# Kernel tuning notes

Measured on AMD Instinct MI355X. Metric: run time of the kernel, lower is better.

Reference implementation:

```python
import jax, jax.numpy as jnp
import numpy as np

N_AST, M, C, D, H, OUT = 200000, 400000, 25000, 256, 4, 256


def setup_inputs() -> dict:
    key = jax.random.key(0)
    ks = jax.random.split(key, 12)
    s = 0.02
    return {
        "ast_nodes_encodings": jax.random.normal(ks[0], (N_AST, D), jnp.float32),
        "ast_node_idx_to_pdg_node_idx_mapping_key": jax.random.randint(ks[1], (M,), 0, N_AST),
        "ast_node_idx_to_pdg_node_idx_mapping_value": jax.random.randint(ks[2], (M,), 0, C),
        "pdg_node_idx_to_sub_ast_root_idx_mapping_key": jax.random.randint(ks[3], (C,), 0, C),
        "pdg_node_idx_to_sub_ast_root_idx_mapping_value": jax.random.randint(ks[4], (C,), 0, N_AST),
        "nr_cfg_nodes": C,
        "Wq": jax.random.normal(ks[5], (D, D), jnp.float32) * s,
        "bq": jnp.zeros((D,), jnp.float32),
        "Wk": jax.random.normal(ks[6], (D, D), jnp.float32) * s,
        "bk": jnp.zeros((D,), jnp.float32),
        "Wv": jax.random.normal(ks[7], (D, D), jnp.float32) * s,
        "bv": jnp.zeros((D,), jnp.float32),
        "Wo": jax.random.normal(ks[8], (D, OUT), jnp.float32) * s,
        "bo": jnp.zeros((OUT,), jnp.float32),
    }


def _scatter_attn(x, attn_keys, seg, num_segments, Wq, bq, Wk, bk, Wv, bv, Wo, bo):
    # x: [M, D] scattered inputs; attn_keys: [C, D] per-segment queries; seg: [M] segment ids.
    d_h = D // H
    q = (attn_keys @ Wq + bq).reshape(num_segments, H, d_h)  # [C,H,dh]
    k = (x @ Wk + bk).reshape(-1, H, d_h)                    # [M,H,dh]
    v = (x @ Wv + bv).reshape(-1, H, d_h)                    # [M,H,dh]
    scale = 1.0 / jnp.sqrt(jnp.asarray(d_h, x.dtype))
    scores = jnp.einsum('mhd,mhd->mh', k, q[seg]) * scale    # [M,H]
    m = jax.ops.segment_max(scores, seg, num_segments=num_segments)  # [C,H]
    e = jnp.exp(scores - m[seg])                             # [M,H]
    denom = jax.ops.segment_sum(e, seg, num_segments=num_segments)  # [C,H]
    num = jax.ops.segment_sum((e[..., None] * v).reshape(-1, H * d_h),
                              seg, num_segments=num_segments)        # [C,D]
    pooled = (num.reshape(num_segments, H, d_h) / (denom[..., None] + 1e-9)).reshape(num_segments, D)
    return pooled @ Wo + bo                                  # [C,OUT]


def reference(ast_nodes_encodings,
              ast_node_idx_to_pdg_node_idx_mapping_key,
              ast_node_idx_to_pdg_node_idx_mapping_value,
              pdg_node_idx_to_sub_ast_root_idx_mapping_key,
              pdg_node_idx_to_sub_ast_root_idx_mapping_value,
              nr_cfg_nodes, Wq, bq, Wk, bk, Wv, bv, Wo, bo):
    # Build per-CFG-node attention keys: gather sub-AST-root encodings, scatter by PDG node idx.
    root_enc = ast_nodes_encodings[pdg_node_idx_to_sub_ast_root_idx_mapping_value]  # [C,D]
    attn_keys = jnp.zeros((nr_cfg_nodes, D), ast_nodes_encodings.dtype)
    attn_keys = attn_keys.at[pdg_node_idx_to_sub_ast_root_idx_mapping_key].set(root_enc)
    # Gather AST node encodings per mapping entry and attention-pool per CFG node.
    scattered = ast_nodes_encodings[ast_node_idx_to_pdg_node_idx_mapping_key]       # [M,D]
    return _scatter_attn(scattered, attn_keys, ast_node_idx_to_pdg_node_idx_mapping_value,
                         nr_cfg_nodes, Wq, bq, Wk, bk, Wv, bv, Wo, bo)
```

## Files before the change

### kernel.cpp

```cpp
#include <hip/hip_runtime.h>
#include <hip/hip_bf16.h>
#include <math.h>

#define D 256
#define H 4
#define DH 64
#define NOUT 256

typedef short bf16x8 __attribute__((ext_vector_type(8)));
typedef float f32x4 __attribute__((ext_vector_type(4)));

__device__ __forceinline__ ushort f2bf(float f){
  uint b = __float_as_uint(f);
  b += 0x7FFF + ((b >> 16) & 1);
  return (ushort)(b >> 16);
}
__device__ __forceinline__ float bf2f(ushort u){
  return __uint_as_float(((uint)u) << 16);
}

__global__ void winner_kernel(const int* __restrict__ key, int* __restrict__ winner, int C){
  int i = blockIdx.x*256 + threadIdx.x;
  if (i < C){ int t = key[i]; if (t >= 0 && t < C) atomicMax(&winner[t], i); }
}

__global__ void count_kernel(const int* __restrict__ seg, int* __restrict__ counts, int M, int C){
  int i = blockIdx.x*256 + threadIdx.x;
  if (i < M){ int s = seg[i]; if (s >= 0 && s < C) atomicAdd(&counts[s], 1); }
}

__global__ __launch_bounds__(1024) void scan1_kernel(const int* __restrict__ counts,
    int* __restrict__ loc, int* __restrict__ btot, int C){
  __shared__ int wtot[16];
  __shared__ int wexcl[16];
  int tid = threadIdx.x, lane = tid & 63, wv = tid >> 6;
  int i = blockIdx.x*1024 + tid;
  int v = (i < C) ? counts[i] : 0;
  int x = v;
  #pragma unroll
  for (int d2 = 1; d2 < 64; d2 <<= 1){
    int t = __shfl_up(x, d2, 64);
    if (lane >= d2) x += t;
  }
  if (lane == 63) wtot[wv] = x;
  __syncthreads();
  if (wv == 0 && lane < 16){
    int t = wtot[lane]; int y = t;
    #pragma unroll
    for (int d2 = 1; d2 < 16; d2 <<= 1){
      int u = __shfl_up(y, d2, 64);
      if (lane >= d2) y += u;
    }
    wexcl[lane] = y - t;
    if (lane == 15) btot[blockIdx.x] = y;
  }
  __syncthreads();
  if (i < C) loc[i] = wexcl[wv] + x - v;
}

__global__ void scan2_kernel(const int* __restrict__ btot, int* __restrict__ bexcl,
                             int nb, int* __restrict__ offsets, int C){
  int lane = threadIdx.x;
  int v = (lane < nb) ? btot[lane] : 0;
  int x = v;
  #pragma unroll
  for (int d2 = 1; d2 < 64; d2 <<= 1){
    int t = __shfl_up(x, d2, 64);
    if (lane >= d2) x += t;
  }
  if (lane < nb) bexcl[lane] = x - v;
  if (lane == 63) offsets[C] = x;
}

__global__ void scan3_kernel(const int* __restrict__ loc, const int* __restrict__ bexcl,
                             int* __restrict__ offsets, int* __restrict__ pos, int C){
  int i = blockIdx.x*256 + threadIdx.x;
  if (i < C){ int o = loc[i] + bexcl[i >> 10]; offsets[i] = o; pos[i] = o; }
}

__global__ void fill_kernel(const int* __restrict__ seg, int* __restrict__ pos,
                            int* __restrict__ members, int M, int C){
  int i = blockIdx.x*256 + threadIdx.x;
  if (i < M){ int s = seg[i]; if (s >= 0 && s < C){ int p = atomicAdd(&pos[s], 1); members[p] = i; } }
}

__global__ void conv3_kernel(const float* __restrict__ Wq, const float* __restrict__ Wk,
                             const float* __restrict__ Wv,
                             ushort* __restrict__ Wq16, ushort* __restrict__ Wk16,
                             ushort* __restrict__ Wv16){
  int id = blockIdx.x*256 + threadIdx.x;
  Wq16[id] = f2bf(Wq[id]);
  Wk16[id] = f2bf(Wk[id]);
  Wv16[id] = f2bf(Wv[id]);
}

__global__ __launch_bounds__(256) void transpose_wo(const float* __restrict__ Wo,
                                                    ushort* __restrict__ WoT16){
  __shared__ float t[64][65];
  int tid = threadIdx.x;
  int r = tid >> 6, cc = tid & 63;
  int bx = blockIdx.x, by = blockIdx.y;
  #pragma unroll
  for (int rr = 0; rr < 64; rr += 4)
    t[rr + r][cc] = Wo[(size_t)(by*64 + rr + r)*256 + bx*64 + cc];
  __syncthreads();
  #pragma unroll
  for (int rr = 0; rr < 64; rr += 4)
    WoT16[(size_t)(bx*64 + rr + r)*256 + by*64 + cc] = f2bf(t[cc][rr + r]);
}

__global__ void prep_small(const float* __restrict__ Wq, const float* __restrict__ Wk,
                           const float* __restrict__ Wo, const float* __restrict__ bq,
                           const float* __restrict__ bk, const float* __restrict__ bv,
                           float* __restrict__ wqbk, float* __restrict__ bvo,
                           float* __restrict__ bqk, float* __restrict__ cbh){
  int id = blockIdx.x*256 + threadIdx.x;
  if (id < 1024){
    int h = id >> 8, k = id & 255;
    float s = 0.f;
    for (int d = 0; d < DH; d++) s += Wq[(size_t)k*256 + h*64 + d] * bk[h*64 + d];
    wqbk[id] = s;
  } else if (id < 2048){
    int t = id - 1024; int h = t >> 8, o = t & 255;
    float s = 0.f;
    for (int d = 0; d < DH; d++) s += bv[h*64 + d] * Wo[(size_t)(h*64 + d)*256 + o];
    bvo[t] = s;
  } else if (id < 3072){
    int t = id - 2048; int h = t >> 8, e = t & 255;
    float s = 0.f;
    for (int d = 0; d < DH; d++) s += bq[h*64 + d] * Wk[(size_t)e*256 + h*64 + d];
    bqk[t] = s;
  } else if (id < 3076){
    int h = id - 3072;
    float s = 0.f;
    for (int d = 0; d < DH; d++) s += bq[h*64 + d] * bk[h*64 + d];
    cbh[h] = s;
  }
}

__global__ void gather_ag(const float* __restrict__ enc, const int* __restrict__ rootval,
                          const int* __restrict__ winner, ushort* __restrict__ Ag, int C){
  int id = blockIdx.x*256 + threadIdx.x;
  if (id < C*64){
    int c = id >> 6, g = id & 63;
    int w = winner[c];
    float4 v = make_float4(0.f, 0.f, 0.f, 0.f);
    if (w >= 0) v = *(const float4*)(enc + (size_t)rootval[w]*D + g*4);
    ushort4 u; u.x = f2bf(v.x); u.y = f2bf(v.y); u.z = f2bf(v.z); u.w = f2bf(v.w);
    *(ushort4*)(Ag + (size_t)c*D + g*4) = u;
  }
}

template<bool OUT_BF16>
__global__ __launch_bounds__(256) void mfma_gemm(
    const ushort* __restrict__ A, int sA, int acol_h,
    const ushort* __restrict__ Bt, int sBt, int btrow_h, int btcol_h,
    void* __restrict__ Out, int sOut, int outrow_h, int outcol_h,
    int M, int K,
    const float* __restrict__ bias, const float* __restrict__ beta4,
    const float* __restrict__ bvo4){
  __shared__ __align__(16) ushort As[64][72];
  __shared__ __align__(16) ushort Bs[64][72];
  int tid = threadIdx.x;
  int hz = blockIdx.z;
  int m0 = blockIdx.x*64;
  int acol0  = acol_h*hz;
  int btrow0 = blockIdx.y*64 + btrow_h*hz;
  int btcol0 = btcol_h*hz;
  int outrow0 = outrow_h*hz;
  int outcol0 = blockIdx.y*64 + outcol_h*hz;
  int w = tid >> 6, lane = tid & 63, quad = lane >> 4, l16 = lane & 15;
  int r1 = tid >> 3, c8 = (tid & 7)*8;
  f32x4 acc[4] = {};
  for (int k0 = 0; k0 < K; k0 += 64){
    const ushort* ga = A + (size_t)(m0 + r1)*sA + acol0 + k0 + c8;
    uint4 v1 = make_uint4(0,0,0,0), v2 = make_uint4(0,0,0,0);
    if (m0 + r1 < M)      v1 = *(const uint4*)ga;
    if (m0 + r1 + 32 < M) v2 = *(const uint4*)(ga + (size_t)32*sA);
    *(uint4*)&As[r1][c8]      = v1;
    *(uint4*)&As[r1+32][c8]   = v2;
    const ushort* gb = Bt + (size_t)(btrow0 + r1)*sBt + btcol0 + k0 + c8;
    *(uint4*)&Bs[r1][c8]      = *(const uint4*)gb;
    *(uint4*)&Bs[r1+32][c8]   = *(const uint4*)(gb + (size_t)32*sBt);
    __syncthreads();
    #pragma unroll
    for (int ks = 0; ks < 2; ks++){
      bf16x8 b = *(const bf16x8*)&Bs[w*16 + l16][ks*32 + quad*8];
      #pragma unroll
      for (int mt = 0; mt < 4; mt++){
        bf16x8 a = *(const bf16x8*)&As[mt*16 + l16][ks*32 + quad*8];
        acc[mt] = __builtin_amdgcn_mfma_f32_16x16x32_bf16(a, b, acc[mt], 0, 0, 0);
      }
    }
    __syncthreads();
  }
  int col = outcol0 + w*16 + l16;
  int bcol = btrow0 + w*16 + l16;
  float bval = bias ? bias[bcol] : 0.f;
  #pragma unroll
  for (int mt = 0; mt < 4; mt++){
    #pragma unroll
    for (int r = 0; r < 4; r++){
      int row = m0 + mt*16 + quad*4 + r;
      if (row < M){
        float v = acc[mt][r] + bval;
        if (bvo4){
          v += beta4[row*4+0]*bvo4[0*256 + bcol] + beta4[row*4+1]*bvo4[1*256 + bcol]
             + beta4[row*4+2]*bvo4[2*256 + bcol] + beta4[row*4+3]*bvo4[3*256 + bcol];
        }
        if (OUT_BF16) ((ushort*)Out)[(size_t)(outrow0 + row)*sOut + col] = f2bf(v);
        else          ((float*)Out)[(size_t)(outrow0 + row)*sOut + col] = v;
      }
    }
  }
}

__global__ __launch_bounds__(256) void seg_attn(const float* __restrict__ enc,
    const int* __restrict__ astkey, const int* __restrict__ members,
    const int* __restrict__ offsets, const ushort* __restrict__ Ag,
    const float* __restrict__ wqbk, const float* __restrict__ cbh,
    const ushort* __restrict__ qk16, ushort* __restrict__ Shat16,
    float* __restrict__ beta, int C){
  int lane = threadIdx.x & 63, wave = threadIdx.x >> 6;
  int c = blockIdx.x*4 + wave;
  if (c >= C) return;
  int half = lane >> 5, sl = lane & 31;
  float qk[4][8];
  const ushort* qkp = qk16 + (size_t)c*1024 + sl*8;
  #pragma unroll
  for (int h = 0; h < 4; h++){
    uint4 u = *(const uint4*)(qkp + h*256);
    qk[h][0]=__uint_as_float(u.x<<16); qk[h][1]=__uint_as_float(u.x&0xffff0000u);
    qk[h][2]=__uint_as_float(u.y<<16); qk[h][3]=__uint_as_float(u.y&0xffff0000u);
    qk[h][4]=__uint_as_float(u.z<<16); qk[h][5]=__uint_as_float(u.z&0xffff0000u);
    qk[h][6]=__uint_as_float(u.w<<16); qk[h][7]=__uint_as_float(u.w&0xffff0000u);
  }
  float qbv[4];
  {
    uint4 a = *(const uint4*)(Ag + (size_t)c*256 + sl*8);
    float av[8];
    av[0]=__uint_as_float(a.x<<16); av[1]=__uint_as_float(a.x&0xffff0000u);
    av[2]=__uint_as_float(a.y<<16); av[3]=__uint_as_float(a.y&0xffff0000u);
    av[4]=__uint_as_float(a.z<<16); av[5]=__uint_as_float(a.z&0xffff0000u);
    av[6]=__uint_as_float(a.w<<16); av[7]=__uint_as_float(a.w&0xffff0000u);
    #pragma unroll
    for (int h = 0; h < 4; h++){
      const float* wp = wqbk + h*256 + sl*8;
      float p = av[0]*wp[0] + av[1]*wp[1] + av[2]*wp[2] + av[3]*wp[3]
              + av[4]*wp[4] + av[5]*wp[5] + av[6]*wp[6] + av[7]*wp[7];
      #pragma unroll
      for (int d2 = 1; d2 < 32; d2 <<= 1) p += __shfl_xor(p, d2, 64);
      qbv[h] = p + cbh[h];
    }
  }
  int off = offsets[c];
  int n = offsets[c+1] - off;
  float S[4][8] = {};
  float l[4] = {0.f, 0.f, 0.f, 0.f};
  for (int base = 0; base < n; base += 64){
    int cnt = min(64, n - base);
    int xrow = 0;
    if (lane < cnt) xrow = astkey[members[off + base + lane]];
    int rA = __shfl(xrow, 0, 64);
    int rB = __shfl(xrow, (cnt > 1) ? 1 : 0, 64);
    int r = half ? rB : rA;
    const float* xp = enc + (size_t)r*256 + sl*8;
    float4 x0 = *(const float4*)xp;
    float4 x1 = *(const float4*)(xp + 4);
    for (int j = 0; j < cnt; j += 2){
      float4 nx0 = x0, nx1 = x1;
      if (j + 2 < cnt){
        int nA = __shfl(xrow, j + 2, 64);
        int nB = __shfl(xrow, (j + 3 < cnt) ? (j + 3) : (j + 2), 64);
        int nr = half ? nB : nA;
        const float* np = enc + (size_t)nr*256 + sl*8;
        nx0 = *(const float4*)np;
        nx1 = *(const float4*)(np + 4);
      }
      float x[8] = {x0.x, x0.y, x0.z, x0.w, x1.x, x1.y, x1.z, x1.w};
      float p[4];
      #pragma unroll
      for (int h = 0; h < 4; h++){
        float s = x[0]*qk[h][0] + x[1]*qk[h][1] + x[2]*qk[h][2] + x[3]*qk[h][3]
                + x[4]*qk[h][4] + x[5]*qk[h][5] + x[6]*qk[h][6] + x[7]*qk[h][7];
        p[h] = s;
      }
      #pragma unroll
      for (int d2 = 1; d2 < 32; d2 <<= 1){
        #pragma unroll
        for (int h = 0; h < 4; h++) p[h] += __shfl_xor(p[h], d2, 64);
      }
      float e[4];
      #pragma unroll
      for (int h = 0; h < 4; h++) e[h] = __expf((p[h] + qbv[h]) * 0.125f);
      if (half & (int)(j + 1 >= cnt)){ e[0] = e[1] = e[2] = e[3] = 0.f; }
      #pragma unroll
      for (int h = 0; h < 4; h++){
        l[h] += e[h];
        #pragma unroll
        for (int k = 0; k < 8; k++) S[h][k] += e[h]*x[k];
      }
      x0 = nx0; x1 = nx1;
    }
  }
  #pragma unroll
  for (int h = 0; h < 4; h++) l[h] += __shfl_xor(l[h], 32, 64);
  #pragma unroll
  for (int h = 0; h < 4; h++){
    #pragma unroll
    for (int k = 0; k < 8; k++) S[h][k] += __shfl_xor(S[h][k], 32, 64);
  }
  float inv[4];
  #pragma unroll
  for (int h = 0; h < 4; h++) inv[h] = 1.f / (l[h] + 1e-9f);
  if (half == 0){
    ushort* sp = Shat16 + (size_t)c*1024 + sl*8;
    #pragma unroll
    for (int h = 0; h < 4; h++){
      float ih = inv[h];
      uint4 o;
      o.x = (uint)f2bf(S[h][0]*ih) | ((uint)f2bf(S[h][1]*ih) << 16);
      o.y = (uint)f2bf(S[h][2]*ih) | ((uint)f2bf(S[h][3]*ih) << 16);
      o.z = (uint)f2bf(S[h][4]*ih) | ((uint)f2bf(S[h][5]*ih) << 16);
      o.w = (uint)f2bf(S[h][6]*ih) | ((uint)f2bf(S[h][7]*ih) << 16);
      *(uint4*)(sp + h*256) = o;
    }
  }
  if (lane == 0){
    beta[c*4+0] = l[0] / (l[0] + 1e-9f);
    beta[c*4+1] = l[1] / (l[1] + 1e-9f);
    beta[c*4+2] = l[2] / (l[2] + 1e-9f);
    beta[c*4+3] = l[3] / (l[3] + 1e-9f);
  }
}

extern "C" void kernel_launch(void* const* d_in, const int* in_sizes, int n_in,
                              void* d_out, int out_size, void* d_ws, size_t ws_size,
                              hipStream_t stream) {
  const float* enc    = (const float*)d_in[0];
  const int*   astkey = (const int*)d_in[1];
  const int*   seg    = (const int*)d_in[2];
  const int*   pdgkey = (const int*)d_in[3];
  const int*   pdgval = (const int*)d_in[4];
  const float* Wq = (const float*)d_in[6];
  const float* bq = (const float*)d_in[7];
  const float* Wk = (const float*)d_in[8];
  const float* bk = (const float*)d_in[9];
  const float* Wv = (const float*)d_in[10];
  const float* bv = (const float*)d_in[11];
  const float* Wo = (const float*)d_in[12];
  const float* bo = (const float*)d_in[13];
  float* out = (float*)d_out;
  const int M = in_sizes[1];
  const int C = in_sizes[3];

  char* p = (char*)d_ws;
  auto alloc = [&](size_t bytes) -> void* {
    void* r = (void*)p;
    p += (bytes + 255) / 256 * 256;
    return r;
  };
  ushort* Ag      = (ushort*)alloc((size_t)C * D * 2);
  ushort* qk16    = (ushort*)alloc((size_t)C * H * D * 2);
  ushort* Shat16  = (ushort*)alloc((size_t)C * H * D * 2);
  float*  beta    = (float*)alloc((size_t)C * H * 4);
  ushort* Wq16    = (ushort*)alloc((size_t)D * D * 2);
  ushort* Wk16    = (ushort*)alloc((size_t)D * D * 2);
  ushort* Wv16    = (ushort*)alloc((size_t)D * D * 2);
  ushort* WoT16   = (ushort*)alloc((size_t)D * D * 2);
  ushort* Gt16    = (ushort*)alloc((size_t)H * D * D * 2);
  ushort* Zt16    = (ushort*)alloc((size_t)D * H * D * 2);
  float*  wqbk    = (float*)alloc((size_t)H * D * 4);
  float*  bvo     = (float*)alloc((size_t)H * NOUT * 4);
  float*  bqk     = (float*)alloc((size_t)H * D * 4);
  float*  cbh     = (float*)alloc((size_t)H * 4);
  int*   winner   = (int*)alloc((size_t)C * 4);
  int*   counts   = (int*)alloc((size_t)C * 4);
  int*   loc      = (int*)alloc((size_t)C * 4);
  int*   btot     = (int*)alloc((size_t)64 * 4);
  int*   bexcl    = (int*)alloc((size_t)64 * 4);
  int*   offsets  = (int*)alloc((size_t)(C + 1) * 4);
  int*   pos      = (int*)alloc((size_t)C * 4);
  int*   members  = (int*)alloc((size_t)M * 4);

  hipMemsetAsync(winner, 0xFF, (size_t)C * 4, stream);
  hipMemsetAsync(counts, 0, (size_t)C * 4, stream);

  int gC = (C + 255) / 256, gM = (M + 255) / 256;
  int nb1024 = (C + 1023) / 1024;
  winner_kernel<<<gC, 256, 0, stream>>>(pdgkey, winner, C);
  count_kernel<<<gM, 256, 0, stream>>>(seg, counts, M, C);
  scan1_kernel<<<nb1024, 1024, 0, stream>>>(counts, loc, btot, C);
  scan2_kernel<<<1, 64, 0, stream>>>(btot, bexcl, nb1024, offsets, C);
  scan3_kernel<<<gC, 256, 0, stream>>>(loc, bexcl, offsets, pos, C);
  fill_kernel<<<gM, 256, 0, stream>>>(seg, pos, members, M, C);

  conv3_kernel<<<(D*D)/256, 256, 0, stream>>>(Wq, Wk, Wv, Wq16, Wk16, Wv16);
  transpose_wo<<<dim3(4,4), 256, 0, stream>>>(Wo, WoT16);
  prep_small<<<13, 256, 0, stream>>>(Wq, Wk, Wo, bq, bk, bv, wqbk, bvo, bqk, cbh);

  mfma_gemm<true><<<dim3(4,4,4), 256, 0, stream>>>(
      Wk16, D, DH,  Wq16, D, 0, DH,  Gt16, D, D, 0,  D, DH, nullptr, nullptr, nullptr);
  mfma_gemm<true><<<dim3(4,4,4), 256, 0, stream>>>(
      WoT16, D, DH,  Wv16, D, 0, DH,  Zt16, H*D, 0, D,  D, DH, nullptr, nullptr, nullptr);

  gather_ag<<<(C*64 + 255)/256, 256, 0, stream>>>(enc, pdgval, winner, Ag, C);

  int mt = (C + 63) / 64;
  mfma_gemm<true><<<dim3(mt,4,4), 256, 0, stream>>>(
      Ag, D, 0,  Gt16, D, D, 0,  qk16, H*D, 0, D,  C, D, bqk, nullptr, nullptr);

  seg_attn<<<(C + 3)/4, 256, 0, stream>>>(enc, astkey, members, offsets, Ag,
                                          wqbk, cbh, qk16, Shat16, beta, C);

  mfma_gemm<false><<<dim3(mt,4,1), 256, 0, stream>>>(
      Shat16, H*D, 0,  Zt16, H*D, 0, 0,  out, NOUT, 0, 0,  C, H*D, bo, beta, bvo);
}
```

Measured before the change: 516.7 us.

## Fuse prep kernels, use DPP reductions, process four rows per segment-attention step

```diff
diff --git a/kernel.cpp b/kernel.cpp
--- a/kernel.cpp
+++ b/kernel.cpp
@@ -15,18 +15,23 @@
   b += 0x7FFF + ((b >> 16) & 1);
   return (ushort)(b >> 16);
 }
-__device__ __forceinline__ float bf2f(ushort u){
-  return __uint_as_float(((uint)u) << 16);
-}
-
-__global__ void winner_kernel(const int* __restrict__ key, int* __restrict__ winner, int C){
-  int i = blockIdx.x*256 + threadIdx.x;
-  if (i < C){ int t = key[i]; if (t >= 0 && t < C) atomicMax(&winner[t], i); }
-}
-
-__global__ void count_kernel(const int* __restrict__ seg, int* __restrict__ counts, int M, int C){
+
+__device__ __forceinline__ float redux32(float v){
+  int t;
+  t = __builtin_amdgcn_update_dpp(0, __float_as_int(v), 0x121, 0xF, 0xF, true); v += __int_as_float(t);
+  t = __builtin_amdgcn_update_dpp(0, __float_as_int(v), 0x122, 0xF, 0xF, true); v += __int_as_float(t);
+  t = __builtin_amdgcn_update_dpp(0, __float_as_int(v), 0x124, 0xF, 0xF, true); v += __int_as_float(t);
+  t = __builtin_amdgcn_update_dpp(0, __float_as_int(v), 0x128, 0xF, 0xF, true); v += __int_as_float(t);
+  v += __shfl_xor(v, 16, 64);
+  return v;
+}
+
+__global__ void count_winner_kernel(const int* __restrict__ seg, int* __restrict__ counts,
+                                    const int* __restrict__ pdgkey, int* __restrict__ winner,
+                                    int M, int C){
   int i = blockIdx.x*256 + threadIdx.x;
   if (i < M){ int s = seg[i]; if (s >= 0 && s < C) atomicAdd(&counts[s], 1); }
+  if (i < C){ int t = pdgkey[i]; if (t >= 0 && t < C) atomicMax(&winner[t], i); }
 }
 
 __global__ __launch_bounds__(1024) void scan1_kernel(const int* __restrict__ counts,
@@ -84,57 +89,56 @@
   if (i < M){ int s = seg[i]; if (s >= 0 && s < C){ int p = atomicAdd(&pos[s], 1); members[p] = i; } }
 }
 
-__global__ void conv3_kernel(const float* __restrict__ Wq, const float* __restrict__ Wk,
-                             const float* __restrict__ Wv,
-                             ushort* __restrict__ Wq16, ushort* __restrict__ Wk16,
-                             ushort* __restrict__ Wv16){
-  int id = blockIdx.x*256 + threadIdx.x;
-  Wq16[id] = f2bf(Wq[id]);
-  Wk16[id] = f2bf(Wk[id]);
-  Wv16[id] = f2bf(Wv[id]);
-}
-
-__global__ __launch_bounds__(256) void transpose_wo(const float* __restrict__ Wo,
-                                                    ushort* __restrict__ WoT16){
+__global__ __launch_bounds__(256) void prep_weights(
+    const float* __restrict__ Wq, const float* __restrict__ Wk,
+    const float* __restrict__ Wv, const float* __restrict__ Wo,
+    const float* __restrict__ bq, const float* __restrict__ bk,
+    const float* __restrict__ bv,
+    ushort* __restrict__ Wq16, ushort* __restrict__ Wk16, ushort* __restrict__ Wv16,
+    ushort* __restrict__ WoT16,
+    float* __restrict__ wqbk, float* __restrict__ bvo,
+    float* __restrict__ bqk, float* __restrict__ cbh){
   __shared__ float t[64][65];
-  int tid = threadIdx.x;
-  int r = tid >> 6, cc = tid & 63;
-  int bx = blockIdx.x, by = blockIdx.y;
-  #pragma unroll
-  for (int rr = 0; rr < 64; rr += 4)
-    t[rr + r][cc] = Wo[(size_t)(by*64 + rr + r)*256 + bx*64 + cc];
-  __syncthreads();
-  #pragma unroll
-  for (int rr = 0; rr < 64; rr += 4)
-    WoT16[(size_t)(bx*64 + rr + r)*256 + by*64 + cc] = f2bf(t[cc][rr + r]);
-}
-
-__global__ void prep_small(const float* __restrict__ Wq, const float* __restrict__ Wk,
-                           const float* __restrict__ Wo, const float* __restrict__ bq,
-                           const float* __restrict__ bk, const float* __restrict__ bv,
-                           float* __restrict__ wqbk, float* __restrict__ bvo,
-                           float* __restrict__ bqk, float* __restrict__ cbh){
-  int id = blockIdx.x*256 + threadIdx.x;
-  if (id < 1024){
-    int h = id >> 8, k = id & 255;
-    float s = 0.f;
-    for (int d = 0; d < DH; d++) s += Wq[(size_t)k*256 + h*64 + d] * bk[h*64 + d];
-    wqbk[id] = s;
-  } else if (id < 2048){
-    int t = id - 1024; int h = t >> 8, o = t & 255;
-    float s = 0.f;
-    for (int d = 0; d < DH; d++) s += bv[h*64 + d] * Wo[(size_t)(h*64 + d)*256 + o];
-    bvo[t] = s;
-  } else if (id < 3072){
-    int t = id - 2048; int h = t >> 8, e = t & 255;
-    float s = 0.f;
-    for (int d = 0; d < DH; d++) s += bq[h*64 + d] * Wk[(size_t)e*256 + h*64 + d];
-    bqk[t] = s;
-  } else if (id < 3076){
-    int h = id - 3072;
-    float s = 0.f;
-    for (int d = 0; d < DH; d++) s += bq[h*64 + d] * bk[h*64 + d];
-    cbh[h] = s;
+  int bid = blockIdx.x, tid = threadIdx.x;
+  if (bid < 256){
+    int id = bid*256 + tid;
+    Wq16[id] = f2bf(Wq[id]);
+    Wk16[id] = f2bf(Wk[id]);
+    Wv16[id] = f2bf(Wv[id]);
+  } else if (bid < 269){
+    int id = (bid - 256)*256 + tid;
+    if (id < 1024){
+      int h = id >> 8, k = id & 255;
+      float s = 0.f;
+      for (int d = 0; d < DH; d++) s += Wq[(size_t)k*256 + h*64 + d] * bk[h*64 + d];
+      wqbk[id] = s;
+    } else if (id < 2048){
+      int tt = id - 1024; int h = tt >> 8, o = tt & 255;
+      float s = 0.f;
+      for (int d = 0; d < DH; d++) s += bv[h*64 + d] * Wo[(size_t)(h*64 + d)*256 + o];
+      bvo[tt] = s;
+    } else if (id < 3072){
+      int tt = id - 2048; int h = tt >> 8, e = tt & 255;
+      float s = 0.f;
+      for (int d = 0; d < DH; d++) s += bq[h*64 + d] * Wk[(size_t)e*256 + h*64 + d];
+      bqk[tt] = s;
+    } else if (id < 3076){
+      int h = id - 3072;
+      float s = 0.f;
+      for (int d = 0; d < DH; d++) s += bq[h*64 + d] * bk[h*64 + d];
+      cbh[h] = s;
+    }
+  } else {
+    int b2 = bid - 269;
+    int bx = b2 & 3, by = b2 >> 2;
+    int r = tid >> 6, cc = tid & 63;
+    #pragma unroll
+    for (int rr = 0; rr < 64; rr += 4)
+      t[rr + r][cc] = Wo[(size_t)(by*64 + rr + r)*256 + bx*64 + cc];
+    __syncthreads();
+    #pragma unroll
+    for (int rr = 0; rr < 64; rr += 4)
+      WoT16[(size_t)(bx*64 + rr + r)*256 + by*64 + cc] = f2bf(t[cc][rr + r]);
   }
 }
 
@@ -248,9 +252,7 @@
       const float* wp = wqbk + h*256 + sl*8;
       float p = av[0]*wp[0] + av[1]*wp[1] + av[2]*wp[2] + av[3]*wp[3]
               + av[4]*wp[4] + av[5]*wp[5] + av[6]*wp[6] + av[7]*wp[7];
-      #pragma unroll
-      for (int d2 = 1; d2 < 32; d2 <<= 1) p += __shfl_xor(p, d2, 64);
-      qbv[h] = p + cbh[h];
+      qbv[h] = redux32(p) + cbh[h];
     }
   }
   int off = offsets[c];
@@ -261,46 +263,53 @@
     int cnt = min(64, n - base);
     int xrow = 0;
     if (lane < cnt) xrow = astkey[members[off + base + lane]];
-    int rA = __shfl(xrow, 0, 64);
-    int rB = __shfl(xrow, (cnt > 1) ? 1 : 0, 64);
-    int r = half ? rB : rA;
-    const float* xp = enc + (size_t)r*256 + sl*8;
-    float4 x0 = *(const float4*)xp;
-    float4 x1 = *(const float4*)(xp + 4);
-    for (int j = 0; j < cnt; j += 2){
-      float4 nx0 = x0, nx1 = x1;
-      if (j + 2 < cnt){
-        int nA = __shfl(xrow, j + 2, 64);
-        int nB = __shfl(xrow, (j + 3 < cnt) ? (j + 3) : (j + 2), 64);
-        int nr = half ? nB : nA;
-        const float* np = enc + (size_t)nr*256 + sl*8;
-        nx0 = *(const float4*)np;
-        nx1 = *(const float4*)(np + 4);
-      }
-      float x[8] = {x0.x, x0.y, x0.z, x0.w, x1.x, x1.y, x1.z, x1.w};
-      float p[4];
+    int r0 = __shfl(xrow, half, 64);
+    int r1 = __shfl(xrow, 2 + half, 64);
+    const float* p0 = enc + (size_t)r0*256 + sl*8;
+    const float* p1 = enc + (size_t)r1*256 + sl*8;
+    float4 xa0 = *(const float4*)p0, xa1 = *(const float4*)(p0 + 4);
+    float4 xb0 = *(const float4*)p1, xb1 = *(const float4*)(p1 + 4);
+    for (int j = 0; j < cnt; j += 4){
+      float4 na0 = xa0, na1 = xa1, nb0 = xb0, nb1 = xb1;
+      if (j + 4 < cnt){
+        int k0 = j + 4 + half, k1 = j + 6 + half;
+        int rr0 = __shfl(xrow, (k0 > 63) ? 63 : k0, 64);
+        int rr1 = __shfl(xrow, (k1 > 63) ? 63 : k1, 64);
+        const float* q0 = enc + (size_t)rr0*256 + sl*8;
+        const float* q1 = enc + (size_t)rr1*256 + sl*8;
+        na0 = *(const float4*)q0; na1 = *(const float4*)(q0 + 4);
+        nb0 = *(const float4*)q1; nb1 = *(const float4*)(q1 + 4);
+      }
+      float xa[8] = {xa0.x, xa0.y, xa0.z, xa0.w, xa1.x, xa1.y, xa1.z, xa1.w};
+      float xb[8] = {xb0.x, xb0.y, xb0.z, xb0.w, xb1.x, xb1.y, xb1.z, xb1.w};
+      float pa[4], pb[4];
       #pragma unroll
       for (int h = 0; h < 4; h++){
-        float s = x[0]*qk[h][0] + x[1]*qk[h][1] + x[2]*qk[h][2] + x[3]*qk[h][3]
-                + x[4]*qk[h][4] + x[5]*qk[h][5] + x[6]*qk[h][6] + x[7]*qk[h][7];
-        p[h] = s;
+        pa[h] = xa[0]*qk[h][0] + xa[1]*qk[h][1] + xa[2]*qk[h][2] + xa[3]*qk[h][3]
+              + xa[4]*qk[h][4] + xa[5]*qk[h][5] + xa[6]*qk[h][6] + xa[7]*qk[h][7];
+        pb[h] = xb[0]*qk[h][0] + xb[1]*qk[h][1] + xb[2]*qk[h][2] + xb[3]*qk[h][3]
+              + xb[4]*qk[h][4] + xb[5]*qk[h][5] + xb[6]*qk[h][6] + xb[7]*qk[h][7];
       }
       #pragma unroll
-      for (int d2 = 1; d2 < 32; d2 <<= 1){
-        #pragma unroll
-        for (int h = 0; h < 4; h++) p[h] += __shfl_xor(p[h], d2, 64);
-      }
-      float e[4];
-      #pragma unroll
-      for (int h = 0; h < 4; h++) e[h] = __expf((p[h] + qbv[h]) * 0.125f);
-      if (half & (int)(j + 1 >= cnt)){ e[0] = e[1] = e[2] = e[3] = 0.f; }
+      for (int h = 0; h < 4; h++){ pa[h] = redux32(pa[h]); pb[h] = redux32(pb[h]); }
+      bool v0 = (j + half) < cnt;
+      bool v1 = (j + 2 + half) < cnt;
+      float ea[4], eb[4];
       #pragma unroll
       for (int h = 0; h < 4; h++){
-        l[h] += e[h];
+        ea[h] = v0 ? __expf((pa[h] + qbv[h]) * 0.125f) : 0.f;
+        eb[h] = v1 ? __expf((pb[h] + qbv[h]) * 0.125f) : 0.f;
+      }
+      #pragma unroll
+      for (int h = 0; h < 4; h++){
+        l[h] += ea[h] + eb[h];
         #pragma unroll
-        for (int k = 0; k < 8; k++) S[h][k] += e[h]*x[k];
-      }
-      x0 = nx0; x1 = nx1;
+        for (int k = 0; k < 8; k++){
+          S[h][k] += ea[h]*xa[k];
+          S[h][k] += eb[h]*xb[k];
+        }
+      }
+      xa0 = na0; xa1 = na1; xb0 = nb0; xb1 = nb1;
     }
   }
   #pragma unroll
@@ -387,17 +396,16 @@
   hipMemsetAsync(counts, 0, (size_t)C * 4, stream);
 
   int gC = (C + 255) / 256, gM = (M + 255) / 256;
+  int gMC = ((M > C ? M : C) + 255) / 256;
   int nb1024 = (C + 1023) / 1024;
-  winner_kernel<<<gC, 256, 0, stream>>>(pdgkey, winner, C);
-  count_kernel<<<gM, 256, 0, stream>>>(seg, counts, M, C);
+  count_winner_kernel<<<gMC, 256, 0, stream>>>(seg, counts, pdgkey, winner, M, C);
   scan1_kernel<<<nb1024, 1024, 0, stream>>>(counts, loc, btot, C);
   scan2_kernel<<<1, 64, 0, stream>>>(btot, bexcl, nb1024, offsets, C);
   scan3_kernel<<<gC, 256, 0, stream>>>(loc, bexcl, offsets, pos, C);
   fill_kernel<<<gM, 256, 0, stream>>>(seg, pos, members, M, C);
 
-  conv3_kernel<<<(D*D)/256, 256, 0, stream>>>(Wq, Wk, Wv, Wq16, Wk16, Wv16);
-  transpose_wo<<<dim3(4,4), 256, 0, stream>>>(Wo, WoT16);
-  prep_small<<<13, 256, 0, stream>>>(Wq, Wk, Wo, bq, bk, bv, wqbk, bvo, bqk, cbh);
+  prep_weights<<<285, 256, 0, stream>>>(Wq, Wk, Wv, Wo, bq, bk, bv,
+                                        Wq16, Wk16, Wv16, WoT16, wqbk, bvo, bqk, cbh);
 
   mfma_gemm<true><<<dim3(4,4,4), 256, 0, stream>>>(
       Wk16, D, DH,  Wq16, D, 0, DH,  Gt16, D, D, 0,  D, DH, nullptr, nullptr, nullptr);
```

Measured after the change: 508.3 us. Within noise of the previous version (-1.6%).
